# Performance work log

Hardware: AMD Instinct MI355X
Metric: run time of the kernel (lower is better)

## Reference

```python
import jax, jax.numpy as jnp
import numpy as np

NUM_CLASSES = 10
CLS_W, L1_W, GIOU_W = 2.0, 5.0, 2.0


def box_cxcywh_to_xyxy(b):
    cx, cy, w, h = b[..., 0], b[..., 1], b[..., 2], b[..., 3]
    return jnp.stack([cx - w / 2, cy - h / 2, cx + w / 2, cy + h / 2], axis=-1)


def giou_matrix(b1, b2):
    # b1: (B,N,4), b2: (B,M,4) xyxy -> (B,N,M)
    a1 = jnp.clip(b1[..., 2] - b1[..., 0], 0) * jnp.clip(b1[..., 3] - b1[..., 1], 0)
    a2 = jnp.clip(b2[..., 2] - b2[..., 0], 0) * jnp.clip(b2[..., 3] - b2[..., 1], 0)
    lt = jnp.maximum(b1[..., :, None, :2], b2[..., None, :, :2])
    rb = jnp.minimum(b1[..., :, None, 2:], b2[..., None, :, 2:])
    wh = jnp.clip(rb - lt, 0)
    inter = wh[..., 0] * wh[..., 1]
    union = a1[..., :, None] + a2[..., None, :] - inter
    iou = inter / jnp.clip(union, 1e-6)
    lte = jnp.minimum(b1[..., :, None, :2], b2[..., None, :, :2])
    rbe = jnp.maximum(b1[..., :, None, 2:], b2[..., None, :, 2:])
    whe = jnp.clip(rbe - lte, 0)
    enc = whe[..., 0] * whe[..., 1]
    return iou - (enc - union) / jnp.clip(enc, 1e-6)


def giou_elem(b1, b2):
    # b1, b2: (N,4) xyxy, paired -> (N,)
    a1 = jnp.clip(b1[:, 2] - b1[:, 0], 0) * jnp.clip(b1[:, 3] - b1[:, 1], 0)
    a2 = jnp.clip(b2[:, 2] - b2[:, 0], 0) * jnp.clip(b2[:, 3] - b2[:, 1], 0)
    lt = jnp.maximum(b1[:, :2], b2[:, :2])
    rb = jnp.minimum(b1[:, 2:], b2[:, 2:])
    wh = jnp.clip(rb - lt, 0)
    inter = wh[:, 0] * wh[:, 1]
    union = a1 + a2 - inter
    iou = inter / jnp.clip(union, 1e-6)
    lte = jnp.minimum(b1[:, :2], b2[:, :2])
    rbe = jnp.maximum(b1[:, 2:], b2[:, 2:])
    whe = jnp.clip(rbe - lte, 0)
    enc = whe[:, 0] * whe[:, 1]
    return iou - (enc - union) / jnp.clip(enc, 1e-6)


def hungarian(cost):
    # Jonker-Volgenant style shortest-augmenting-path assignment (== scipy.linear_sum_assignment)
    cost = np.asarray(cost, dtype=np.float64)
    transposed = cost.shape[0] > cost.shape[1]
    C = cost.T if transposed else cost
    n, m = C.shape  # n <= m
    u = np.zeros(n + 1)
    v = np.zeros(m + 1)
    p = np.zeros(m + 1, dtype=np.int64)
    colr = np.arange(m + 1)
    for i in range(1, n + 1):
        p[0] = i
        j0 = 0
        minv = np.full(m + 1, np.inf)
        way = np.zeros(m + 1, dtype=np.int64)
        used = np.zeros(m + 1, dtype=bool)
        while True:
            used[j0] = True
            i0 = p[j0]
            unused = colr[1:][~used[1:]]
            cur = C[i0 - 1, unused - 1] - u[i0] - v[unused]
            better = cur < minv[unused]
            bidx = unused[better]
            minv[bidx] = cur[better]
            way[bidx] = j0
            j1 = unused[np.argmin(minv[unused])]
            delta = minv[j1]
            u[p[used]] += delta
            v[used] -= delta
            minv[~used] -= delta
            j0 = j1
            if p[j0] == 0:
                break
        while j0 != 0:
            jn = way[j0]
            p[j0] = p[jn]
            j0 = jn
    rows = p[1:] - 1
    cols = np.arange(m)
    sel = rows >= 0
    r, c = rows[sel], cols[sel]
    if transposed:
        r, c = c, r
    order = np.argsort(r)
    return r[order], c[order]


def compute_matches(pred_logits, pred_boxes, gt_classes, gt_boxes):
    # Batched cost matrices on device, per-sample Hungarian on host (mirrors torch.no_grad matcher).
    B, Q, _ = pred_logits.shape
    G = gt_classes.shape[1]
    prob = jax.nn.softmax(pred_logits, axis=-1)
    cls_idx = jnp.clip(gt_classes, 0, NUM_CLASSES - 1)
    idx = jnp.broadcast_to(cls_idx[:, None, :], (B, Q, G))
    cls_cost = -jnp.take_along_axis(prob, idx, axis=2)                 # (B,Q,G)
    l1_cost = jnp.abs(pred_boxes[:, :, None, :] - gt_boxes[:, None, :, :]).sum(-1)
    g = giou_matrix(box_cxcywh_to_xyxy(pred_boxes), box_cxcywh_to_xyxy(gt_boxes))
    cost = CLS_W * cls_cost + L1_W * l1_cost - GIOU_W * g
    cost_np = np.asarray(jax.device_get(cost))
    valid_np = np.asarray(jax.device_get(gt_classes)) >= 0
    bs, ps, gs = [], [], []
    for bi in range(B):
        vidx = np.nonzero(valid_np[bi])[0]
        if vidx.size == 0:
            continue
        r, c = hungarian(cost_np[bi][:, vidx])
        bs.append(np.full(r.size, bi, dtype=np.int64))
        ps.append(r.astype(np.int64))
        gs.append(vidx[c].astype(np.int64))
    if bs:
        return np.concatenate(bs), np.concatenate(ps), np.concatenate(gs)
    z = np.zeros(0, np.int64)
    return z, z, z


def detection_loss(pred_logits, pred_boxes, gt_boxes, target_cls, b_f, p_f, g_f, n_matched):
    C1 = pred_logits.shape[-1]
    logp = jax.nn.log_softmax(pred_logits, axis=-1).reshape(-1, C1)
    t = target_cls.reshape(-1)
    w = jnp.ones(C1, dtype=pred_logits.dtype).at[-1].set(0.1)
    nll = -jnp.take_along_axis(logp, t[:, None], axis=1)[:, 0]
    wt = w[t]
    cls_loss = (wt * nll).sum() / wt.sum()
    mp = pred_boxes[b_f, p_f]
    mg = gt_boxes[b_f, g_f]
    l1 = jnp.abs(mp - mg).sum()
    gd = giou_elem(box_cxcywh_to_xyxy(mp), box_cxcywh_to_xyxy(mg))
    gl = (1.0 - gd).sum()
    return CLS_W * cls_loss + L1_W * l1 / n_matched + GIOU_W * gl / n_matched


def setup_inputs() -> dict:
    key = jax.random.key(0)
    k1, k2, k3, k4, k5 = jax.random.split(key, 5)
    B, Q, G, C = 64, 900, 100, NUM_CLASSES
    pred_logits = jax.random.normal(k1, (B, Q, C + 1), dtype=jnp.float32)
    pred_boxes = jax.random.uniform(k2, (B, Q, 4), dtype=jnp.float32, minval=0.05, maxval=0.6)
    gt_boxes = jax.random.uniform(k3, (B, G, 4), dtype=jnp.float32, minval=0.05, maxval=0.6)
    cls = jax.random.randint(k4, (B, G), 0, C)
    nvalid = jax.random.randint(k5, (B,), 1, G + 1)
    mask = jnp.arange(G)[None, :] < nvalid[:, None]
    gt_classes = jnp.where(mask, cls, -1).astype(jnp.int32)
    return {"pred_logits": pred_logits, "pred_boxes": pred_boxes,
            "gt_classes": gt_classes, "gt_boxes": gt_boxes}


def reference(pred_logits, pred_boxes, gt_classes, gt_boxes):
    B, Q = pred_logits.shape[:2]
    b_f, p_f, g_f = compute_matches(pred_logits, pred_boxes, gt_classes, gt_boxes)
    gt_np = np.asarray(jax.device_get(gt_classes))
    tc = np.full((B, Q), NUM_CLASSES, dtype=np.int32)
    tc[b_f, p_f] = gt_np[b_f, g_f]
    n_matched = max(int(b_f.size), 1)
    return detection_loss(pred_logits, pred_boxes, gt_boxes, jnp.asarray(tc), b_f, p_f, g_f, n_matched)
```

## Files before the change

kernel.cpp:

```cpp
#include <hip/hip_runtime.h>
#include <hip/hip_bf16.h>
#include <math.h>

#define BB 64
#define QQ 900
#define GG 100
#define NCLS 10
#define CP1 11

#define STRIDE 960
#define KPL 15
#define NT 512
#define NW 8
#define QMASK 255
#define ROUND_CAP 20000

#define CLS_W 2.0f
#define L1_W 5.0f
#define GIOU_W 2.0f

struct Accum {
  double wnll, wt, l1, gl;
  int nm, counter;
  int pad[6];
};

__global__ __launch_bounds__(256) void cost_kernel(
    const float* __restrict__ logits, const float* __restrict__ pboxes,
    const int* __restrict__ gcls, const float* __restrict__ gboxes,
    float* __restrict__ cost, Accum* acc) {
  const int b = blockIdx.y;
  const int q = blockIdx.x * 256 + threadIdx.x;

  if (blockIdx.x == 0 && blockIdx.y == 0 && threadIdx.x == 0) {
    acc->wnll = 0.0; acc->wt = 0.0; acc->l1 = 0.0; acc->gl = 0.0;
    acc->nm = 0; acc->counter = 0;
  }

  __shared__ float s_gb[GG * 4];
  __shared__ int   s_gc[GG];
  __shared__ float s_prob[256 * 13];

  for (int i = threadIdx.x; i < GG * 4; i += 256) s_gb[i] = gboxes[b * GG * 4 + i];
  for (int i = threadIdx.x; i < GG; i += 256)     s_gc[i] = gcls[b * GG + i];

  float pcx = 0.f, pcy = 0.f, pw = 0.f, ph = 0.f;
  if (q < QQ) {
    const float* lg = logits + ((size_t)b * QQ + q) * CP1;
    float l[CP1];
    float mx = -1e30f;
    for (int c = 0; c < CP1; ++c) { l[c] = lg[c]; mx = fmaxf(mx, l[c]); }
    float se = 0.f;
    for (int c = 0; c < CP1; ++c) { l[c] = expf(l[c] - mx); se += l[c]; }
    float inv = 1.0f / se;
    for (int c = 0; c < CP1; ++c) s_prob[threadIdx.x * 13 + c] = l[c] * inv;
    const float* pb = pboxes + ((size_t)b * QQ + q) * 4;
    pcx = pb[0]; pcy = pb[1]; pw = pb[2]; ph = pb[3];
  }
  __syncthreads();
  if (q >= STRIDE) return;

  float* crow = cost + ((size_t)b * GG) * STRIDE + q;
  if (q >= QQ) {
    for (int g = 0; g < GG; ++g) crow[(size_t)g * STRIDE] = 1e30f;
    return;
  }

  const float px1 = pcx - 0.5f * pw, py1 = pcy - 0.5f * ph;
  const float px2 = pcx + 0.5f * pw, py2 = pcy + 0.5f * ph;
  const float pa = fmaxf(px2 - px1, 0.f) * fmaxf(py2 - py1, 0.f);

  for (int g = 0; g < GG; ++g) {
    int cls = s_gc[g];
    cls = cls < 0 ? 0 : (cls > NCLS - 1 ? NCLS - 1 : cls);
    const float cc = -s_prob[threadIdx.x * 13 + cls];
    const float gcx = s_gb[g * 4 + 0], gcy = s_gb[g * 4 + 1];
    const float gw  = s_gb[g * 4 + 2], gh  = s_gb[g * 4 + 3];
    const float l1 = fabsf(pcx - gcx) + fabsf(pcy - gcy) + fabsf(pw - gw) + fabsf(ph - gh);
    const float gx1 = gcx - 0.5f * gw, gy1 = gcy - 0.5f * gh;
    const float gx2 = gcx + 0.5f * gw, gy2 = gcy + 0.5f * gh;
    const float ga = fmaxf(gx2 - gx1, 0.f) * fmaxf(gy2 - gy1, 0.f);
    const float ltx = fmaxf(px1, gx1), lty = fmaxf(py1, gy1);
    const float rbx = fminf(px2, gx2), rby = fminf(py2, gy2);
    const float iw = fmaxf(rbx - ltx, 0.f), ih = fmaxf(rby - lty, 0.f);
    const float inter = iw * ih;
    const float uni = pa + ga - inter;
    const float iou = inter / fmaxf(uni, 1e-6f);
    const float ex1 = fminf(px1, gx1), ey1 = fminf(py1, gy1);
    const float ex2 = fmaxf(px2, gx2), ey2 = fmaxf(py2, gy2);
    const float ew = fmaxf(ex2 - ex1, 0.f), eh = fmaxf(ey2 - ey1, 0.f);
    const float enc = ew * eh;
    const float giou = iou - (enc - uni) / fmaxf(enc, 1e-6f);
    crow[(size_t)g * STRIDE] = CLS_W * cc + L1_W * l1 - GIOU_W * giou;
  }
}

__global__ __launch_bounds__(NT) void jv_kernel(
    const float* __restrict__ logits, const float* __restrict__ pboxes,
    const int* __restrict__ gcls, const float* __restrict__ gboxes,
    const float* __restrict__ cost, Accum* acc, float* out) {
  const int b = blockIdx.x;
  const int tid = threadIdx.x;
  const int lane = tid & 63;
  const int w = tid >> 6;

  __shared__ float vl[STRIDE + 2];
  __shared__ int   p[QQ + 1];
  __shared__ unsigned long long way64[STRIDE + 2];
  __shared__ float m1l[GG + 1], m2l[GG + 1];
  __shared__ int   aminl[GG + 1];
  __shared__ int   s_gc[GG];
  __shared__ int   queue[QMASK + 1];
  __shared__ int   sh_n, sh_qtail;
  __shared__ double r0[NW], r1[NW], r2[NW], r3[NW];
  __shared__ int r4[NW];

  if (tid == 0) { sh_n = 0; sh_qtail = 0; }
  for (int j = tid; j <= QQ; j += NT) p[j] = 0;
  for (int j = tid; j < STRIDE + 2; j += NT) { vl[j] = 0.f; way64[j] = 0ull; }
  if (tid < GG) s_gc[tid] = gcls[b * GG + tid];
  __syncthreads();
  if (tid < GG && s_gc[tid] >= 0) atomicAdd(&sh_n, 1);
  __syncthreads();
  const int n = sh_n;
  const float* Cb = cost + (size_t)b * GG * STRIDE;

  for (int r = w; r < n; r += NW) {
    const float* Cr = Cb + (size_t)r * STRIDE + lane;
    float rca[KPL];
#pragma unroll
    for (int k = 0; k < KPL; ++k) rca[k] = Cr[k << 6];
    float m1 = 3e38f, m2 = 3e38f, n1 = 3e38f, n2 = 3e38f;
    int j1 = 0x7FFFFFFF, i1 = 0x7FFFFFFF;
#pragma unroll
    for (int k = 0; k < 8; ++k) {
      const float c = rca[k];
      if (c < m1) { m2 = m1; m1 = c; j1 = 1 + lane + (k << 6); }
      else if (c < m2) m2 = c;
    }
#pragma unroll
    for (int k = 8; k < KPL; ++k) {
      const float c = rca[k];
      if (c < n1) { n2 = n1; n1 = c; i1 = 1 + lane + (k << 6); }
      else if (c < n2) n2 = c;
    }
    if (n1 < m1) { m2 = fminf(m1, n2); m1 = n1; j1 = i1; }
    else m2 = fminf(m2, n1);
    for (int m = 1; m < 64; m <<= 1) {
      const float o1 = __shfl_xor(m1, m);
      const float o2 = __shfl_xor(m2, m);
      const int oj = __shfl_xor(j1, m);
      if (o1 < m1) { m2 = fminf(m1, o2); m1 = o1; j1 = oj; }
      else m2 = fminf(m2, o1);
    }
    if (lane == 0) { m1l[r] = m1; m2l[r] = m2; aminl[r] = j1; }
  }
  __syncthreads();

  if (tid < n) {
    const float regret = m2l[tid] - m1l[tid];
    const unsigned long long key =
        ((unsigned long long)__float_as_uint(regret) << 20) | (unsigned long long)(tid + 1);
    atomicMax(&way64[aminl[tid]], key);
  }
  __syncthreads();
  if (tid < n) {
    const int j1 = aminl[tid];
    if ((int)(way64[j1] & 0xFFFFFu) == tid + 1) {
      p[j1] = tid + 1;
      vl[j1] = m1l[tid] - m2l[tid];
    } else {
      const int t0 = atomicAdd(&sh_qtail, 1);
      queue[t0 & QMASK] = tid + 1;
    }
  }
  __syncthreads();

  if (w == 0) {
    float v[KPL];
#pragma unroll
    for (int k = 0; k < KPL; ++k) v[k] = vl[1 + lane + (k << 6)];
    int head = 0, tail = sh_qtail, rounds = 0;

    float bufA[KPL], bufB[KPL], bufC[KPL];
    int ia = -1, ib = -1, ic = -1;

    auto loadrow = [&](float* buf, int rid) {
      const float* Cr = Cb + (size_t)(rid - 1) * STRIDE + lane;
#pragma unroll
      for (int k = 0; k < KPL; ++k) buf[k] = Cr[k << 6];
    };
    auto do_step = [&](float* rc, int i) {
      float m1 = 3e38f, m2 = 3e38f, n1 = 3e38f, n2 = 3e38f;
      int j1 = 0x7FFFFFFF, i1 = 0x7FFFFFFF;
#pragma unroll
      for (int k = 0; k < 8; ++k) {
        const float c = rc[k] - v[k];
        if (c < m1) { m2 = m1; m1 = c; j1 = 1 + lane + (k << 6); }
        else if (c < m2) m2 = c;
      }
#pragma unroll
      for (int k = 8; k < KPL; ++k) {
        const float c = rc[k] - v[k];
        if (c < n1) { n2 = n1; n1 = c; i1 = 1 + lane + (k << 6); }
        else if (c < n2) n2 = c;
      }
      if (n1 < m1) { m2 = fminf(m1, n2); m1 = n1; j1 = i1; }
      else m2 = fminf(m2, n1);
      for (int m = 1; m < 64; m <<= 1) {
        const float o1 = __shfl_xor(m1, m);
        const float o2 = __shfl_xor(m2, m);
        const int oj = __shfl_xor(j1, m);
        if (o1 < m1) { m2 = fminf(m1, o2); m1 = o1; j1 = oj; }
        else m2 = fminf(m2, o1);
      }
      float d = m2 - m1;
      if (d < 0.f) d = 0.f;
      const int c0 = j1 - 1;
      if ((c0 & 63) == lane) {
        const int kk = c0 >> 6;
        const float ov = v[kk];
        float nv = ov - d;
        if (!(nv < ov)) nv = nextafterf(ov, -3e38f);
        v[kk] = nv;
      }
      const int k0 = p[j1];
      p[j1] = i;
      head++;
      if (k0 > 0) {
        if (lane == 0) queue[tail & QMASK] = k0;
        tail++;
      }
    };

    if (head < tail)     { ia = queue[head & QMASK];       loadrow(bufA, ia); }
    if (head + 1 < tail) { ib = queue[(head + 1) & QMASK]; loadrow(bufB, ib); }
    if (head + 2 < tail) { ic = queue[(head + 2) & QMASK]; loadrow(bufC, ic); }

    while (head < tail && rounds < ROUND_CAP) {
      if (ia < 0) { ia = queue[head & QMASK]; loadrow(bufA, ia); }
      do_step(bufA, ia);
      ia = -1;
      if (head + 2 < tail) { ia = queue[(head + 2) & QMASK]; loadrow(bufA, ia); }
      rounds++;
      if (!(head < tail && rounds < ROUND_CAP)) break;
      if (ib < 0) { ib = queue[head & QMASK]; loadrow(bufB, ib); }
      do_step(bufB, ib);
      ib = -1;
      if (head + 2 < tail) { ib = queue[(head + 2) & QMASK]; loadrow(bufB, ib); }
      rounds++;
      if (!(head < tail && rounds < ROUND_CAP)) break;
      if (ic < 0) { ic = queue[head & QMASK]; loadrow(bufC, ic); }
      do_step(bufC, ic);
      ic = -1;
      if (head + 2 < tail) { ic = queue[(head + 2) & QMASK]; loadrow(bufC, ic); }
      rounds++;
    }
  }
  __syncthreads();

  double wnll = 0.0, wt = 0.0, l1d = 0.0, gld = 0.0;
  int nm = 0;
  for (int q = tid; q < QQ; q += NT) {
    const int idx = b * QQ + q;
    const float* lg = logits + (size_t)idx * CP1;
    float l[CP1];
    float mx = -1e30f;
    for (int c = 0; c < CP1; ++c) { l[c] = lg[c]; mx = fmaxf(mx, l[c]); }
    float se = 0.f;
    for (int c = 0; c < CP1; ++c) se += expf(l[c] - mx);
    const float lse = logf(se);
    const int g = p[q + 1] - 1;
    const int t = (g >= 0) ? s_gc[g] : NCLS;
    float lt = l[0];
    for (int c = 1; c < CP1; ++c) lt = (c == t) ? l[c] : lt;
    const float logp = (lt - mx) - lse;
    const float wgt = (t == NCLS) ? 0.1f : 1.0f;
    wnll += (double)(wgt * (-logp));
    wt += (double)wgt;
    if (g >= 0) {
      nm += 1;
      const float* pb = pboxes + (size_t)idx * 4;
      const float* gb = gboxes + ((size_t)b * GG + g) * 4;
      const float pcx = pb[0], pcy = pb[1], pw = pb[2], ph = pb[3];
      const float gcx = gb[0], gcy = gb[1], gw = gb[2], gh = gb[3];
      const float l1 = fabsf(pcx - gcx) + fabsf(pcy - gcy) + fabsf(pw - gw) + fabsf(ph - gh);
      const float px1 = pcx - 0.5f * pw, py1 = pcy - 0.5f * ph;
      const float px2 = pcx + 0.5f * pw, py2 = pcy + 0.5f * ph;
      const float gx1 = gcx - 0.5f * gw, gy1 = gcy - 0.5f * gh;
      const float gx2 = gcx + 0.5f * gw, gy2 = gcy + 0.5f * gh;
      const float pa = fmaxf(px2 - px1, 0.f) * fmaxf(py2 - py1, 0.f);
      const float ga = fmaxf(gx2 - gx1, 0.f) * fmaxf(gy2 - gy1, 0.f);
      const float ltx = fmaxf(px1, gx1), lty = fmaxf(py1, gy1);
      const float rbx = fminf(px2, gx2), rby = fminf(py2, gy2);
      const float iw = fmaxf(rbx - ltx, 0.f), ih = fmaxf(rby - lty, 0.f);
      const float inter = iw * ih;
      const float uni = pa + ga - inter;
      const float iou = inter / fmaxf(uni, 1e-6f);
      const float ex1 = fminf(px1, gx1), ey1 = fminf(py1, gy1);
      const float ex2 = fmaxf(px2, gx2), ey2 = fmaxf(py2, gy2);
      const float ew = fmaxf(ex2 - ex1, 0.f), eh = fmaxf(ey2 - ey1, 0.f);
      const float enc = ew * eh;
      const float giou = iou - (enc - uni) / fmaxf(enc, 1e-6f);
      l1d += (double)l1;
      gld += (double)(1.0f - giou);
    }
  }

  for (int off = 32; off; off >>= 1) {
    wnll += __shfl_down(wnll, off);
    wt   += __shfl_down(wt, off);
    l1d  += __shfl_down(l1d, off);
    gld  += __shfl_down(gld, off);
    nm   += __shfl_down(nm, off);
  }
  if (lane == 0) { r0[w] = wnll; r1[w] = wt; r2[w] = l1d; r3[w] = gld; r4[w] = nm; }
  __syncthreads();
  if (tid == 0) {
    for (int x = 1; x < NW; ++x) { wnll += r0[x]; wt += r1[x]; l1d += r2[x]; gld += r3[x]; nm += r4[x]; }
    atomicAdd(&acc->wnll, wnll);
    atomicAdd(&acc->wt, wt);
    atomicAdd(&acc->l1, l1d);
    atomicAdd(&acc->gl, gld);
    atomicAdd(&acc->nm, nm);
    __threadfence();
    const int ticket = atomicAdd(&acc->counter, 1);
    if (ticket == BB - 1) {
      const double fw = atomicAdd(&acc->wnll, 0.0);
      const double fwt = atomicAdd(&acc->wt, 0.0);
      const double fl1 = atomicAdd(&acc->l1, 0.0);
      const double fgl = atomicAdd(&acc->gl, 0.0);
      int fnm = atomicAdd(&acc->nm, 0);
      if (fnm < 1) fnm = 1;
      const double loss = (double)CLS_W * (fw / fwt) +
                          ((double)L1_W * fl1 + (double)GIOU_W * fgl) / (double)fnm;
      out[0] = (float)loss;
    }
  }
}

extern "C" void kernel_launch(void* const* d_in, const int* in_sizes, int n_in,
                              void* d_out, int out_size, void* d_ws, size_t ws_size,
                              hipStream_t stream) {
  const float* logits = (const float*)d_in[0];
  const float* pboxes = (const float*)d_in[1];
  const int*   gcls   = (const int*)d_in[2];
  const float* gboxes = (const float*)d_in[3];

  char* ws = (char*)d_ws;
  Accum* acc = (Accum*)ws;
  float* cost = (float*)(ws + 128);

  cost_kernel<<<dim3((STRIDE + 255) / 256, BB), 256, 0, stream>>>(logits, pboxes, gcls, gboxes, cost, acc);
  jv_kernel<<<BB, NT, 0, stream>>>(logits, pboxes, gcls, gboxes, cost, acc, (float*)d_out);
}
```

Before: 117.6 us.

## Fuse per-row min/second-min into cost kernel and overlap softmax with JV solve

The cost kernel now splits each batch into 128-query chunks with two halves of the GT rows per block. Each block stages its cost tile in shared memory and writes per-chunk row min, second-min and argmin partials, and it skips rows past the valid GT count. The JV kernel merges 8 partials per row instead of rescanning the whole cost matrix. Idle warps precompute the log-sum-exp of the logits while warp 0 runs the augmenting loop, so the loss stage reads only one logit per query. This removes a global re-read and a softmax pass from the serial tail, at the cost of more shared memory and extra partial buffers. Cost rows past n are no longer written, which depends on the JV loop never reading them.

```diff
diff --git a/kernel.cpp b/kernel.cpp
--- a/kernel.cpp
+++ b/kernel.cpp
@@ -15,6 +15,9 @@
 #define QMASK 255
 #define ROUND_CAP 20000
 
+#define NCH 8
+#define QCH 128
+
 #define CLS_W 2.0f
 #define L1_W 5.0f
 #define GIOU_W 2.0f
@@ -28,77 +31,118 @@
 __global__ __launch_bounds__(256) void cost_kernel(
     const float* __restrict__ logits, const float* __restrict__ pboxes,
     const int* __restrict__ gcls, const float* __restrict__ gboxes,
-    float* __restrict__ cost, Accum* acc) {
+    float* __restrict__ cost, float4* __restrict__ part, Accum* acc) {
   const int b = blockIdx.y;
-  const int q = blockIdx.x * 256 + threadIdx.x;
-
-  if (blockIdx.x == 0 && blockIdx.y == 0 && threadIdx.x == 0) {
+  const int chunk = blockIdx.x;
+  const int tid = threadIdx.x;
+  const int ql = tid & (QCH - 1);
+  const int gh = tid >> 7;
+  const int q = chunk * QCH + ql;
+
+  if (chunk == 0 && b == 0 && tid == 0) {
     acc->wnll = 0.0; acc->wt = 0.0; acc->l1 = 0.0; acc->gl = 0.0;
     acc->nm = 0; acc->counter = 0;
   }
 
   __shared__ float s_gb[GG * 4];
   __shared__ int   s_gc[GG];
-  __shared__ float s_prob[256 * 13];
-
-  for (int i = threadIdx.x; i < GG * 4; i += 256) s_gb[i] = gboxes[b * GG * 4 + i];
-  for (int i = threadIdx.x; i < GG; i += 256)     s_gc[i] = gcls[b * GG + i];
+  __shared__ float s_prob[QCH * 13];
+  __shared__ float s_c[GG][QCH + 1];
+  __shared__ int   sh_n;
+
+  if (tid == 0) sh_n = 0;
+  __syncthreads();
+
+  for (int i = tid; i < GG * 4; i += 256) s_gb[i] = gboxes[b * GG * 4 + i];
+  for (int i = tid; i < GG; i += 256) {
+    const int v = gcls[b * GG + i];
+    s_gc[i] = v;
+    if (v >= 0) atomicAdd(&sh_n, 1);
+  }
 
   float pcx = 0.f, pcy = 0.f, pw = 0.f, ph = 0.f;
   if (q < QQ) {
-    const float* lg = logits + ((size_t)b * QQ + q) * CP1;
-    float l[CP1];
-    float mx = -1e30f;
-    for (int c = 0; c < CP1; ++c) { l[c] = lg[c]; mx = fmaxf(mx, l[c]); }
-    float se = 0.f;
-    for (int c = 0; c < CP1; ++c) { l[c] = expf(l[c] - mx); se += l[c]; }
-    float inv = 1.0f / se;
-    for (int c = 0; c < CP1; ++c) s_prob[threadIdx.x * 13 + c] = l[c] * inv;
     const float* pb = pboxes + ((size_t)b * QQ + q) * 4;
     pcx = pb[0]; pcy = pb[1]; pw = pb[2]; ph = pb[3];
-  }
-  __syncthreads();
-  if (q >= STRIDE) return;
-
-  float* crow = cost + ((size_t)b * GG) * STRIDE + q;
-  if (q >= QQ) {
-    for (int g = 0; g < GG; ++g) crow[(size_t)g * STRIDE] = 1e30f;
-    return;
-  }
+    if (gh == 0) {
+      const float* lg = logits + ((size_t)b * QQ + q) * CP1;
+      float l[CP1];
+      float mx = -1e30f;
+      for (int c = 0; c < CP1; ++c) { l[c] = lg[c]; mx = fmaxf(mx, l[c]); }
+      float se = 0.f;
+      for (int c = 0; c < CP1; ++c) { l[c] = expf(l[c] - mx); se += l[c]; }
+      const float inv = 1.0f / se;
+      for (int c = 0; c < NCLS; ++c) s_prob[ql * 13 + c] = l[c] * inv;
+    }
+  }
+  __syncthreads();
+  const int sn = sh_n;
 
   const float px1 = pcx - 0.5f * pw, py1 = pcy - 0.5f * ph;
   const float px2 = pcx + 0.5f * pw, py2 = pcy + 0.5f * ph;
   const float pa = fmaxf(px2 - px1, 0.f) * fmaxf(py2 - py1, 0.f);
 
-  for (int g = 0; g < GG; ++g) {
-    int cls = s_gc[g];
-    cls = cls < 0 ? 0 : (cls > NCLS - 1 ? NCLS - 1 : cls);
-    const float cc = -s_prob[threadIdx.x * 13 + cls];
-    const float gcx = s_gb[g * 4 + 0], gcy = s_gb[g * 4 + 1];
-    const float gw  = s_gb[g * 4 + 2], gh  = s_gb[g * 4 + 3];
-    const float l1 = fabsf(pcx - gcx) + fabsf(pcy - gcy) + fabsf(pw - gw) + fabsf(ph - gh);
-    const float gx1 = gcx - 0.5f * gw, gy1 = gcy - 0.5f * gh;
-    const float gx2 = gcx + 0.5f * gw, gy2 = gcy + 0.5f * gh;
-    const float ga = fmaxf(gx2 - gx1, 0.f) * fmaxf(gy2 - gy1, 0.f);
-    const float ltx = fmaxf(px1, gx1), lty = fmaxf(py1, gy1);
-    const float rbx = fminf(px2, gx2), rby = fminf(py2, gy2);
-    const float iw = fmaxf(rbx - ltx, 0.f), ih = fmaxf(rby - lty, 0.f);
-    const float inter = iw * ih;
-    const float uni = pa + ga - inter;
-    const float iou = inter / fmaxf(uni, 1e-6f);
-    const float ex1 = fminf(px1, gx1), ey1 = fminf(py1, gy1);
-    const float ex2 = fmaxf(px2, gx2), ey2 = fmaxf(py2, gy2);
-    const float ew = fmaxf(ex2 - ex1, 0.f), eh = fmaxf(ey2 - ey1, 0.f);
-    const float enc = ew * eh;
-    const float giou = iou - (enc - uni) / fmaxf(enc, 1e-6f);
-    crow[(size_t)g * STRIDE] = CLS_W * cc + L1_W * l1 - GIOU_W * giou;
+  float* crow = cost + ((size_t)b * GG) * STRIDE + q;
+  const int g0 = gh * 50;
+  const int gend = (g0 + 50 < sn) ? g0 + 50 : sn;
+  for (int g = g0; g < gend; ++g) {
+    float cv = 3e38f;
+    if (q < QQ) {
+      int cls = s_gc[g];
+      cls = cls < 0 ? 0 : (cls > NCLS - 1 ? NCLS - 1 : cls);
+      const float cc = -s_prob[ql * 13 + cls];
+      const float gcx = s_gb[g * 4 + 0], gcy = s_gb[g * 4 + 1];
+      const float gw  = s_gb[g * 4 + 2], gh2 = s_gb[g * 4 + 3];
+      const float l1 = fabsf(pcx - gcx) + fabsf(pcy - gcy) + fabsf(pw - gw) + fabsf(ph - gh2);
+      const float gx1 = gcx - 0.5f * gw, gy1 = gcy - 0.5f * gh2;
+      const float gx2 = gcx + 0.5f * gw, gy2 = gcy + 0.5f * gh2;
+      const float ga = fmaxf(gx2 - gx1, 0.f) * fmaxf(gy2 - gy1, 0.f);
+      const float ltx = fmaxf(px1, gx1), lty = fmaxf(py1, gy1);
+      const float rbx = fminf(px2, gx2), rby = fminf(py2, gy2);
+      const float iw = fmaxf(rbx - ltx, 0.f), ih = fmaxf(rby - lty, 0.f);
+      const float inter = iw * ih;
+      const float uni = pa + ga - inter;
+      const float iou = inter / fmaxf(uni, 1e-6f);
+      const float ex1 = fminf(px1, gx1), ey1 = fminf(py1, gy1);
+      const float ex2 = fmaxf(px2, gx2), ey2 = fmaxf(py2, gy2);
+      const float ew = fmaxf(ex2 - ex1, 0.f), eh = fmaxf(ey2 - ey1, 0.f);
+      const float enc = ew * eh;
+      const float giou = iou - (enc - uni) / fmaxf(enc, 1e-6f);
+      cv = CLS_W * cc + L1_W * l1 - GIOU_W * giou;
+      crow[(size_t)g * STRIDE] = cv;
+    } else if (q < STRIDE) {
+      crow[(size_t)g * STRIDE] = 1e30f;
+    }
+    s_c[g][ql] = cv;
+  }
+  __syncthreads();
+
+  if (tid < sn) {
+    const int kmax = (chunk == NCH - 1) ? (QQ - (NCH - 1) * QCH) : QCH;
+    float m1 = 3e38f, m2 = 3e38f, n1 = 3e38f, n2 = 3e38f;
+    int j1 = 0x7FFFFFFF, i1 = 0x7FFFFFFF;
+    const int ka = kmax < 64 ? kmax : 64;
+    for (int k = 0; k < ka; ++k) {
+      const float c = s_c[tid][k];
+      if (c < m1) { m2 = m1; m1 = c; j1 = 1 + chunk * QCH + k; }
+      else if (c < m2) m2 = c;
+    }
+    for (int k = 64; k < kmax; ++k) {
+      const float c = s_c[tid][k];
+      if (c < n1) { n2 = n1; n1 = c; i1 = 1 + chunk * QCH + k; }
+      else if (c < n2) n2 = c;
+    }
+    if (n1 < m1) { m2 = fminf(m1, n2); m1 = n1; j1 = i1; }
+    else m2 = fminf(m2, n1);
+    part[((size_t)b * NCH + chunk) * QCH + tid] = make_float4(m1, m2, __int_as_float(j1), 0.f);
   }
 }
 
 __global__ __launch_bounds__(NT) void jv_kernel(
     const float* __restrict__ logits, const float* __restrict__ pboxes,
     const int* __restrict__ gcls, const float* __restrict__ gboxes,
-    const float* __restrict__ cost, Accum* acc, float* out) {
+    const float* __restrict__ cost, const float4* __restrict__ part,
+    Accum* acc, float* out) {
   const int b = blockIdx.x;
   const int tid = threadIdx.x;
   const int lane = tid & 63;
@@ -114,6 +158,7 @@
   __shared__ int   sh_n, sh_qtail;
   __shared__ double r0[NW], r1[NW], r2[NW], r3[NW];
   __shared__ int r4[NW];
+  __shared__ float s_lse[QQ], s_mx[QQ];
 
   if (tid == 0) { sh_n = 0; sh_qtail = 0; }
   for (int j = tid; j <= QQ; j += NT) p[j] = 0;
@@ -125,35 +170,17 @@
   const int n = sh_n;
   const float* Cb = cost + (size_t)b * GG * STRIDE;
 
-  for (int r = w; r < n; r += NW) {
-    const float* Cr = Cb + (size_t)r * STRIDE + lane;
-    float rca[KPL];
-#pragma unroll
-    for (int k = 0; k < KPL; ++k) rca[k] = Cr[k << 6];
-    float m1 = 3e38f, m2 = 3e38f, n1 = 3e38f, n2 = 3e38f;
-    int j1 = 0x7FFFFFFF, i1 = 0x7FFFFFFF;
-#pragma unroll
-    for (int k = 0; k < 8; ++k) {
-      const float c = rca[k];
-      if (c < m1) { m2 = m1; m1 = c; j1 = 1 + lane + (k << 6); }
-      else if (c < m2) m2 = c;
-    }
-#pragma unroll
-    for (int k = 8; k < KPL; ++k) {
-      const float c = rca[k];
-      if (c < n1) { n2 = n1; n1 = c; i1 = 1 + lane + (k << 6); }
-      else if (c < n2) n2 = c;
-    }
-    if (n1 < m1) { m2 = fminf(m1, n2); m1 = n1; j1 = i1; }
-    else m2 = fminf(m2, n1);
-    for (int m = 1; m < 64; m <<= 1) {
-      const float o1 = __shfl_xor(m1, m);
-      const float o2 = __shfl_xor(m2, m);
-      const int oj = __shfl_xor(j1, m);
-      if (o1 < m1) { m2 = fminf(m1, o2); m1 = o1; j1 = oj; }
-      else m2 = fminf(m2, o1);
-    }
-    if (lane == 0) { m1l[r] = m1; m2l[r] = m2; aminl[r] = j1; }
+  for (int r = tid; r < n; r += NT) {
+    float m1 = 3e38f, m2 = 3e38f;
+    int j1 = 0x7FFFFFFF;
+#pragma unroll
+    for (int ch = 0; ch < NCH; ++ch) {
+      const float4 pr = part[((size_t)b * NCH + ch) * QCH + r];
+      const float pm1 = pr.x, pm2 = pr.y;
+      if (pm1 < m1) { m2 = fminf(m1, pm2); m1 = pm1; j1 = __float_as_int(pr.z); }
+      else m2 = fminf(m2, pm1);
+    }
+    m1l[r] = m1; m2l[r] = m2; aminl[r] = j1;
   }
   __syncthreads();
 
@@ -256,6 +283,17 @@
       if (head + 2 < tail) { ic = queue[(head + 2) & QMASK]; loadrow(bufC, ic); }
       rounds++;
     }
+  } else {
+    for (int qq = tid - 64; qq < QQ; qq += (NT - 64)) {
+      const float* lg = logits + ((size_t)b * QQ + qq) * CP1;
+      float l[CP1];
+      float mx = -1e30f;
+      for (int c = 0; c < CP1; ++c) { l[c] = lg[c]; mx = fmaxf(mx, l[c]); }
+      float se = 0.f;
+      for (int c = 0; c < CP1; ++c) se += expf(l[c] - mx);
+      s_mx[qq] = mx;
+      s_lse[qq] = logf(se);
+    }
   }
   __syncthreads();
 
@@ -263,18 +301,10 @@
   int nm = 0;
   for (int q = tid; q < QQ; q += NT) {
     const int idx = b * QQ + q;
-    const float* lg = logits + (size_t)idx * CP1;
-    float l[CP1];
-    float mx = -1e30f;
-    for (int c = 0; c < CP1; ++c) { l[c] = lg[c]; mx = fmaxf(mx, l[c]); }
-    float se = 0.f;
-    for (int c = 0; c < CP1; ++c) se += expf(l[c] - mx);
-    const float lse = logf(se);
     const int g = p[q + 1] - 1;
     const int t = (g >= 0) ? s_gc[g] : NCLS;
-    float lt = l[0];
-    for (int c = 1; c < CP1; ++c) lt = (c == t) ? l[c] : lt;
-    const float logp = (lt - mx) - lse;
+    const float lt = logits[(size_t)idx * CP1 + t];
+    const float logp = (lt - s_mx[q]) - s_lse[q];
     const float wgt = (t == NCLS) ? 0.1f : 1.0f;
     wnll += (double)(wgt * (-logp));
     wt += (double)wgt;
@@ -349,8 +379,9 @@
 
   char* ws = (char*)d_ws;
   Accum* acc = (Accum*)ws;
-  float* cost = (float*)(ws + 128);
-
-  cost_kernel<<<dim3((STRIDE + 255) / 256, BB), 256, 0, stream>>>(logits, pboxes, gcls, gboxes, cost, acc);
-  jv_kernel<<<BB, NT, 0, stream>>>(logits, pboxes, gcls, gboxes, cost, acc, (float*)d_out);
+  float4* part = (float4*)(ws + 4096);
+  float* cost = (float*)(ws + 4096 + (size_t)BB * NCH * QCH * sizeof(float4));
+
+  cost_kernel<<<dim3(NCH, BB), 256, 0, stream>>>(logits, pboxes, gcls, gboxes, cost, part, acc);
+  jv_kernel<<<BB, NT, 0, stream>>>(logits, pboxes, gcls, gboxes, cost, part, acc, (float*)d_out);
 }
```

New measurement: 114.6 us. 2.6% less time.
